# Optimization experiments

Measured on AMD Instinct MI355X. Metric: run time of the kernel, lower is better.

## Reference

```python
import jax, jax.numpy as jnp
import numpy as np

MID = 128
N_STAGES = 5  # 224 -> 110 -> 53 -> 25 -> 11 -> 4 (conv3 valid + maxpool3 s2)
EPS_SN = 1e-12


def conv2d(x, w, b, ):
    y = jax.lax.conv_general_dilated(x, w, (1, 1), [(0, 0), (0, 0)],
                                     dimension_numbers=('NCHW', 'OIHW', 'NCHW'))
    return y + b[None, :, None, None]


def maxpool3s2(x):
    return jax.lax.reduce_window(x, -jnp.inf, jax.lax.max,
                                 (1, 1, 3, 3), (1, 1, 2, 2), 'VALID')


def batchnorm(x, g, b, eps=1e-5):
    mu = x.mean(axis=(0, 2, 3), keepdims=True)
    var = x.var(axis=(0, 2, 3), keepdims=True)  # biased, training-mode BN
    return (x - mu) * jax.lax.rsqrt(var + eps) * g[None, :, None, None] + b[None, :, None, None]


def lrn(x, size, alpha=1e-4, beta=0.75, k=1.0):
    # matches F.local_response_norm: zero-padded channel window average of x^2
    sq = x * x
    pad_l, pad_r = size // 2, (size - 1) // 2
    p = jnp.pad(sq, ((0, 0), (pad_l, pad_r), (0, 0), (0, 0)))
    cs = jnp.cumsum(p, axis=1)
    cs = jnp.concatenate([jnp.zeros_like(cs[:, :1]), cs], axis=1)
    win = cs[:, size:] - cs[:, :-size]  # (N,C,H,W) windowed sums
    return x / (k + alpha * win / size) ** beta


def spectral_normalize(theta, u0, v0):
    # u,v carry sequentially across the batch, as in the original python loop
    def nrm(z):
        return z / jnp.maximum(jnp.linalg.norm(z), EPS_SN)

    def step(carry, W):
        u, v = carry
        for _ in range(4):
            v = nrm(W.T @ u)
            u = nrm(W @ v)
        sigma = u @ (W @ v)
        return (u, v), W / sigma

    _, out = jax.lax.scan(step, (u0, v0), theta)
    return out


def affine_grid(theta, H, W):
    # align_corners=False pixel-center normalized coords
    xs = (jnp.arange(W, dtype=theta.dtype) * 2 + 1) / W - 1
    ys = (jnp.arange(H, dtype=theta.dtype) * 2 + 1) / H - 1
    gy, gx = jnp.meshgrid(ys, xs, indexing='ij')
    base = jnp.stack([gx, gy, jnp.ones_like(gx)], axis=-1)  # (H,W,3)
    return jnp.einsum('nij,hwj->nhwi', theta, base)  # (N,H,W,2), last dim (x,y)


def _reflect(x, size):
    # reflection padding over [-0.5, size-0.5], then clip (align_corners=False)
    x = jnp.abs(x + 0.5) % (2.0 * size)
    x = jnp.where(x > size, 2.0 * size - x, x)
    return jnp.clip(x - 0.5, 0.0, size - 1.0)


def grid_sample_reflect(img, grid):
    N, C, H, W = img.shape
    ix = _reflect(((grid[..., 0] + 1) * W - 1) * 0.5, W)
    iy = _reflect(((grid[..., 1] + 1) * H - 1) * 0.5, H)
    x0 = jnp.floor(ix); y0 = jnp.floor(iy)
    wx = ix - x0; wy = iy - y0
    x0i = jnp.clip(x0.astype(jnp.int32), 0, W - 1)
    y0i = jnp.clip(y0.astype(jnp.int32), 0, H - 1)
    x1i = jnp.clip(x0.astype(jnp.int32) + 1, 0, W - 1)
    y1i = jnp.clip(y0.astype(jnp.int32) + 1, 0, H - 1)

    def one(im, y0i, x0i, y1i, x1i, wx, wy):  # im: (C,H,W)
        return (im[:, y0i, x0i] * ((1 - wx) * (1 - wy))[None]
                + im[:, y0i, x1i] * (wx * (1 - wy))[None]
                + im[:, y1i, x0i] * ((1 - wx) * wy)[None]
                + im[:, y1i, x1i] * (wx * wy)[None])

    return jax.vmap(one)(img, y0i, x0i, y1i, x1i, wx, wy)


def forward(x, conv0_w, conv0_b, convs_w, convs_b, bn_g, bn_b, Wr, br, u0, v0):
    N, C, H, W = x.shape
    xs = jax.nn.relu(batchnorm(conv2d(x, conv0_w, conv0_b), bn_g[0], bn_b[0]))
    for i in range(N_STAGES):
        xs = conv2d(xs, convs_w[i], convs_b[i])
        xs = maxpool3s2(xs)
        xs = jax.nn.relu(batchnorm(xs, bn_g[i + 1], bn_b[i + 1]))
    xs = lrn(xs, MID)
    xs = xs.reshape(N, -1)
    reg = xs @ Wr.T + br  # (N,7)
    theta = reg[:, 0:6].reshape(-1, 2, 3)
    m = jax.nn.sigmoid(reg[:, 6])
    theta = spectral_normalize(theta, u0, v0)
    grid = affine_grid(theta, H, W)
    xout = grid_sample_reflect(x, grid)
    return xout * m[:, None, None, None]


def setup_inputs() -> dict:
    key = jax.random.key(0)
    ks = jax.random.split(key, 12)
    N, C, H, W = 16, 16, 224, 224
    x = jax.random.normal(ks[0], (N, C, H, W), dtype=jnp.float32)
    conv0_w = jax.random.normal(ks[1], (MID, C, 1, 1), dtype=jnp.float32) * 0.05
    conv0_b = jax.random.normal(ks[2], (MID,), dtype=jnp.float32) * 0.01
    convs_w = jax.random.normal(ks[3], (N_STAGES, MID, MID, 3, 3), dtype=jnp.float32) * 0.03
    convs_b = jax.random.normal(ks[4], (N_STAGES, MID), dtype=jnp.float32) * 0.01
    bn_g = jnp.ones((N_STAGES + 1, MID), dtype=jnp.float32)
    bn_b = jnp.zeros((N_STAGES + 1, MID), dtype=jnp.float32)
    feat = MID * 4 * 4  # final spatial 4x4
    Wr = jax.random.normal(ks[5], (7, feat), dtype=jnp.float32) * 0.01
    br = jnp.concatenate([jnp.array([1, 0, 0, 0, 1, 0], dtype=jnp.float32),
                          jax.random.normal(ks[6], (1,), dtype=jnp.float32) * 0.1])
    u0 = jax.random.normal(ks[7], (2,), dtype=jnp.float32)
    u0 = u0 / jnp.maximum(jnp.linalg.norm(u0), EPS_SN)
    v0 = jax.random.normal(ks[8], (3,), dtype=jnp.float32)
    v0 = v0 / jnp.maximum(jnp.linalg.norm(v0), EPS_SN)
    return {"x": x, "conv0_w": conv0_w, "conv0_b": conv0_b, "convs_w": convs_w,
            "convs_b": convs_b, "bn_g": bn_g, "bn_b": bn_b, "Wr": Wr, "br": br,
            "u0": u0, "v0": v0}


def reference(x, conv0_w, conv0_b, convs_w, convs_b, bn_g, bn_b, Wr, br, u0, v0):
    return forward(x, conv0_w, conv0_b, convs_w, convs_b, bn_g, bn_b, Wr, br, u0, v0)
```

## Files before the change

kernel.cpp:

```cpp
#include <hip/hip_runtime.h>
#include <math.h>


#define CO_PB 8
#define PLANE 1216

__device__ __forceinline__ void gld_lds4(const float* g, float* l) {
  __builtin_amdgcn_global_load_lds(
      (const __attribute__((address_space(1))) void*)(g),
      (__attribute__((address_space(3))) void*)(l), 4, 0, 0);
}

__global__ void zero_kernel(float* __restrict__ p, int n) {
  int i = blockIdx.x * 256 + threadIdx.x;
  if (i < n) p[i] = 0.f;
}

__global__ __launch_bounds__(256) void moment_kernel(
    const float* __restrict__ x, float* __restrict__ mom) {
  const int tid = threadIdx.x;
  int q = blockIdx.x * 256 + tid;
  int n = q / 12544, pq = q - n * 12544;
  const float* xb = x + ((long)n * 16) * 50176 + pq * 4;
  float4 v4[16];
#pragma unroll
  for (int i = 0; i < 16; ++i) v4[i] = *(const float4*)(xb + (long)i * 50176);
  float accs[16];
  float accp[136];
#pragma unroll
  for (int i = 0; i < 16; ++i) accs[i] = 0.f;
#pragma unroll
  for (int k = 0; k < 136; ++k) accp[k] = 0.f;
#pragma unroll
  for (int p = 0; p < 4; ++p) {
    float v[16];
#pragma unroll
    for (int i = 0; i < 16; ++i)
      v[i] = (p == 0) ? v4[i].x : (p == 1) ? v4[i].y : (p == 2) ? v4[i].z : v4[i].w;
#pragma unroll
    for (int i = 0; i < 16; ++i) accs[i] += v[i];
    int k = 0;
#pragma unroll
    for (int i = 0; i < 16; ++i)
#pragma unroll
      for (int j = i; j < 16; ++j) { accp[k] += v[i] * v[j]; ++k; }
  }
  __shared__ float s_part[4][152];
  const int lane = tid & 63, wv = tid >> 6;
#pragma unroll
  for (int k = 0; k < 16; ++k) {
    float t = accs[k];
#pragma unroll
    for (int o = 32; o; o >>= 1) t += __shfl_down(t, o, 64);
    if (lane == 0) s_part[wv][k] = t;
  }
#pragma unroll
  for (int k = 0; k < 136; ++k) {
    float t = accp[k];
#pragma unroll
    for (int o = 32; o; o >>= 1) t += __shfl_down(t, o, 64);
    if (lane == 0) s_part[wv][16 + k] = t;
  }
  __syncthreads();
  if (tid < 152) {
    float t = s_part[0][tid] + s_part[1][tid] + s_part[2][tid] + s_part[3][tid];
    atomicAdd(&mom[tid], t);
  }
}

__global__ void foldbn_kernel(const float* __restrict__ w0,
                              const float* __restrict__ mom,
                              const float* __restrict__ g,
                              const float* __restrict__ b,
                              float* __restrict__ Wp, float* __restrict__ bp) {
  int c = threadIdx.x;
  if (c >= 128) return;
  const float invN = 1.f / 802816.f;
  float w[16], m[16];
#pragma unroll
  for (int i = 0; i < 16; ++i) { w[i] = w0[c * 16 + i]; m[i] = mom[i] * invN; }
  float mu = 0.f;
#pragma unroll
  for (int i = 0; i < 16; ++i) mu += w[i] * m[i];
  float ey2 = 0.f;
  int k = 0;
#pragma unroll
  for (int i = 0; i < 16; ++i)
#pragma unroll
    for (int j = i; j < 16; ++j) {
      float Mij = mom[16 + k] * invN;
      ey2 += ((i == j) ? 1.f : 2.f) * w[i] * w[j] * Mij;
      ++k;
    }
  float var = ey2 - mu * mu;
  float al = g[c] * rsqrtf(var + 1e-5f);
#pragma unroll
  for (int i = 0; i < 16; ++i) Wp[c * 16 + i] = al * w[i];
  bp[c] = b[c] - al * mu;
}

__global__ __launch_bounds__(256) void conv0act_kernel(
    const float* __restrict__ x, const float* __restrict__ Wp,
    const float* __restrict__ bp, float* __restrict__ act, int n_base) {
  __shared__ float sw[512];
  __shared__ float sb[32];
  const int tid = threadIdx.x;
  const int co0 = blockIdx.y * 32;
  for (int e = tid; e < 512; e += 256) sw[e] = Wp[co0 * 16 + e];
  if (tid < 32) sb[tid] = bp[co0 + tid];
  __syncthreads();
  const int q = blockIdx.x * 256 + tid;
  const int nloc = blockIdx.z;
  const float* xb = x + ((long)(n_base + nloc) * 16) * 50176 + q * 4;
  float4 v4[16];
#pragma unroll
  for (int i = 0; i < 16; ++i) v4[i] = *(const float4*)(xb + (long)i * 50176);
  float* ob = act + ((long)nloc * 128) * 50176 + q * 4;
  for (int u = 0; u < 32; ++u) {
    float bb = sb[u];
    float4 a = make_float4(bb, bb, bb, bb);
#pragma unroll
    for (int i = 0; i < 16; ++i) {
      float w = sw[u * 16 + i];
      a.x += w * v4[i].x; a.y += w * v4[i].y;
      a.z += w * v4[i].z; a.w += w * v4[i].w;
    }
    a.x = fmaxf(a.x, 0.f); a.y = fmaxf(a.y, 0.f);
    a.z = fmaxf(a.z, 0.f); a.w = fmaxf(a.w, 0.f);
    *(float4*)(ob + (long)(co0 + u) * 50176) = a;
  }
}

__global__ __launch_bounds__(256) void stats_kernel(
    const float* __restrict__ buf, float* __restrict__ stats, int P2) {
  const int c = blockIdx.x;
  const int n = blockIdx.y;
  const int tid = threadIdx.x;
  const float* b = buf + ((long)n * 128 + c) * P2;
  float s = 0.f, q = 0.f;
  for (int i = tid; i < P2; i += 256) {
    float v = b[i];
    s += v; q += v * v;
  }
  __shared__ float rs[256], rq[256];
  rs[tid] = s; rq[tid] = q;
  __syncthreads();
  for (int off = 128; off; off >>= 1) {
    if (tid < off) { rs[tid] += rs[tid + off]; rq[tid] += rq[tid + off]; }
    __syncthreads();
  }
  if (tid == 0) {
    atomicAdd(&stats[c], rs[0]);
    atomicAdd(&stats[128 + c], rq[0]);
  }
}

__global__ __launch_bounds__(256) void bnrelu_kernel(
    float* __restrict__ buf, const float* __restrict__ stats,
    const float* __restrict__ g, const float* __restrict__ b,
    int P2, float invM, long total) {
  long i = (long)blockIdx.x * 256 + threadIdx.x;
  if (i >= total) return;
  int c = (int)((i / P2) & 127);
  float mu = stats[c] * invM;
  float var = stats[128 + c] * invM - mu * mu;
  float al = g[c] * rsqrtf(var + 1e-5f);
  float v = buf[i];
  buf[i] = fmaxf(al * (v - mu) + b[c], 0.f);
}

__global__ __launch_bounds__(256, 4) void conv3pool_kernel(
    const float* __restrict__ in, const float* __restrict__ wt,
    float* __restrict__ out, int Sin, int Pout, int n_base) {
  const int tid = threadIdx.x;
  const int tilesX = (Pout + 14) / 15;
  const int ty = blockIdx.x / tilesX, tx = blockIdx.x - ty * tilesX;
  const int co0 = blockIdx.y * CO_PB;
  const int nloc = blockIdx.z;
  const int py0 = ty * 15, px0 = tx * 15;
  const int iy0 = py0 * 2, ix0 = px0 * 2;

  __shared__ __align__(16) float s_in[4 * PLANE];
  __shared__ __align__(16) float s_wt[4][CO_PB][12];

  const int pi = tid >> 4, pj = tid & 15;

  int off[5];
#pragma unroll
  for (int j = 0; j < 5; ++j) {
    int e2 = tid + 256 * j;
    int r = e2 / 34, cc = e2 - 34 * r;
    int gy = iy0 + r; if (gy > Sin - 1) gy = Sin - 1;
    int gx = ix0 + cc; if (gx > Sin - 1) gx = Sin - 1;
    off[j] = gy * Sin + gx;
  }

  int wg0, wl0, wg1, wl1;
  {
    int e = tid;
    int cil = e / 72, rem = e - 72 * cil, u = rem / 9, t = rem - 9 * u;
    wg0 = ((co0 + u) * 128 + cil) * 9 + t;
    wl0 = (cil * CO_PB + u) * 12 + t;
    e = tid + 256;
    cil = e / 72; rem = e - 72 * cil; u = rem / 9; t = rem - 9 * u;
    wg1 = ((co0 + u) * 128 + cil) * 9 + t;
    wl1 = (cil * CO_PB + u) * 12 + t;
  }

  float acc[CO_PB][4];
#pragma unroll
  for (int u = 0; u < CO_PB; ++u)
#pragma unroll
    for (int k = 0; k < 4; ++k) acc[u][k] = 0.f;

  const long S2 = (long)Sin * Sin;
  const float* inN = in + ((long)nloc * 128) * S2;
  const int wb = tid & 192;

  for (int ci0 = 0; ci0 < 128; ci0 += 4) {
    __syncthreads();

    float w0v = wt[wg0 + 9 * ci0];
    float w1v = 0.f;
    if (tid < 32) w1v = wt[wg1 + 9 * ci0];

#pragma unroll
    for (int cil = 0; cil < 4; ++cil) {
      const float* src = inN + (long)(ci0 + cil) * S2;
      float* dplane = &s_in[cil * PLANE + wb];
#pragma unroll
      for (int j = 0; j < 4; ++j) gld_lds4(src + off[j], dplane + j * 256);
      if (tid < 192) gld_lds4(src + off[4], dplane + 4 * 256);
    }

    ((float*)s_wt)[wl0] = w0v;
    if (tid < 32) ((float*)s_wt)[wl1] = w1v;
    __syncthreads();

#pragma unroll
    for (int cil = 0; cil < 4; ++cil) {
      const float* ip = &s_in[cil * PLANE] + (2 * pi) * 34 + 2 * pj;
      float iv[16];
#pragma unroll
      for (int r = 0; r < 4; ++r) {
        float2 a = *(const float2*)(ip + r * 34);
        float2 b = *(const float2*)(ip + r * 34 + 2);
        iv[r * 4 + 0] = a.x; iv[r * 4 + 1] = a.y;
        iv[r * 4 + 2] = b.x; iv[r * 4 + 3] = b.y;
      }
#pragma unroll
      for (int u = 0; u < CO_PB; ++u) {
        const float4* wq = (const float4*)&s_wt[cil][u][0];
        float4 q0 = wq[0], q1 = wq[1], q2 = wq[2];
        float wv[9] = {q0.x, q0.y, q0.z, q0.w, q1.x, q1.y, q1.z, q1.w, q2.x};
#pragma unroll
        for (int ky = 0; ky < 3; ++ky)
#pragma unroll
          for (int kx = 0; kx < 3; ++kx) {
            float w = wv[ky * 3 + kx];
            acc[u][0] += w * iv[ky * 4 + kx];
            acc[u][1] += w * iv[ky * 4 + kx + 1];
            acc[u][2] += w * iv[(ky + 1) * 4 + kx];
            acc[u][3] += w * iv[(ky + 1) * 4 + kx + 1];
          }
      }
    }
  }

  float* s_conv = s_in;
  const int gpy = py0 + pi, gpx = px0 + pj;
  const bool wvalid = (pi < 15) && (pj < 15) && (gpy < Pout) && (gpx < Pout);
  float* cp = s_conv + (2 * pi) * 33 + 2 * pj;
  const float* rp = s_conv + (2 * pi) * 33 + 2 * pj;
#pragma unroll
  for (int u = 0; u < CO_PB; ++u) {
    __syncthreads();
    cp[0] = acc[u][0]; cp[1] = acc[u][1];
    cp[33] = acc[u][2]; cp[34] = acc[u][3];
    __syncthreads();
    if (wvalid) {
      float mx = rp[0];
#pragma unroll
      for (int dy = 0; dy < 3; ++dy)
#pragma unroll
        for (int dx = 0; dx < 3; ++dx)
          mx = fmaxf(mx, rp[dy * 33 + dx]);
      out[(((long)(n_base + nloc) * 128 + (co0 + u)) * Pout + gpy) * Pout + gpx] = mx;
    }
  }
}

__global__ __launch_bounds__(128) void lrn_kernel(float* __restrict__ buf) {
  const int n = blockIdx.x;
  const int c = threadIdx.x;
  __shared__ float sq[128];
  float* b = buf + (long)n * 2048;
  for (int p = 0; p < 16; ++p) {
    float v = b[c * 16 + p];
    sq[c] = v * v;
    __syncthreads();
    int lo = c - 64 < 0 ? 0 : c - 64;
    int hi = c + 63 > 127 ? 127 : c + 63;
    float win = 0.f;
    for (int j = lo; j <= hi; ++j) win += sq[j];
    b[c * 16 + p] = v * powf(1.f + (1e-4f / 128.f) * win, -0.75f);
    __syncthreads();
  }
}

__global__ __launch_bounds__(256) void gemv_kernel(
    const float* __restrict__ xs, const float* __restrict__ Wr,
    const float* __restrict__ br, float* __restrict__ reg) {
  const int n = blockIdx.x;
  const int tid = threadIdx.x;
  float a[7] = {0.f, 0.f, 0.f, 0.f, 0.f, 0.f, 0.f};
  for (int e = tid; e < 2048; e += 256) {
    float v = xs[(long)n * 2048 + e];
#pragma unroll
    for (int j = 0; j < 7; ++j) a[j] += v * Wr[j * 2048 + e];
  }
  __shared__ float red[256];
  for (int j = 0; j < 7; ++j) {
    red[tid] = a[j];
    __syncthreads();
    for (int off = 128; off; off >>= 1) {
      if (tid < off) red[tid] += red[tid + off];
      __syncthreads();
    }
    if (tid == 0) reg[n * 7 + j] = red[0] + br[j];
    __syncthreads();
  }
}

__global__ void sn_kernel(const float* __restrict__ reg,
                          const float* __restrict__ u0g,
                          const float* __restrict__ v0g,
                          float* __restrict__ theta, float* __restrict__ m) {
  if (threadIdx.x != 0 || blockIdx.x != 0) return;
  float u[2] = {u0g[0], u0g[1]};
  float v[3] = {v0g[0], v0g[1], v0g[2]};
  for (int n = 0; n < 16; ++n) {
    const float* W = reg + n * 7;
    for (int it = 0; it < 4; ++it) {
      float v0n = W[0] * u[0] + W[3] * u[1];
      float v1n = W[1] * u[0] + W[4] * u[1];
      float v2n = W[2] * u[0] + W[5] * u[1];
      float nv = sqrtf(v0n * v0n + v1n * v1n + v2n * v2n);
      nv = fmaxf(nv, 1e-12f);
      v[0] = v0n / nv; v[1] = v1n / nv; v[2] = v2n / nv;
      float u0n = W[0] * v[0] + W[1] * v[1] + W[2] * v[2];
      float u1n = W[3] * v[0] + W[4] * v[1] + W[5] * v[2];
      float nu = sqrtf(u0n * u0n + u1n * u1n);
      nu = fmaxf(nu, 1e-12f);
      u[0] = u0n / nu; u[1] = u1n / nu;
    }
    float Wv0 = W[0] * v[0] + W[1] * v[1] + W[2] * v[2];
    float Wv1 = W[3] * v[0] + W[4] * v[1] + W[5] * v[2];
    float sigma = u[0] * Wv0 + u[1] * Wv1;
    for (int k = 0; k < 6; ++k) theta[n * 6 + k] = W[k] / sigma;
    m[n] = 1.f / (1.f + expf(-W[6]));
  }
}

__device__ __forceinline__ float reflectf(float x, float size) {
  x = fabsf(x + 0.5f);
  x = fmodf(x, 2.f * size);
  if (x > size) x = 2.f * size - x;
  x -= 0.5f;
  return fminf(fmaxf(x, 0.f), size - 1.f);
}

__global__ __launch_bounds__(256) void sample_kernel(
    const float* __restrict__ x, const float* __restrict__ theta,
    const float* __restrict__ m, float* __restrict__ out) {
  long i = (long)blockIdx.x * 256 + threadIdx.x;
  if (i >= 12845056L) return;
  int w = (int)(i % 224);
  long t = i / 224;
  int h = (int)(t % 224); t /= 224;
  int c = (int)(t % 16);
  int n = (int)(t / 16);
  const float* th = theta + n * 6;
  float xn = (2 * w + 1) * (1.f / 224.f) - 1.f;
  float yn = (2 * h + 1) * (1.f / 224.f) - 1.f;
  float gx = th[0] * xn + th[1] * yn + th[2];
  float gy = th[3] * xn + th[4] * yn + th[5];
  float ix = reflectf(((gx + 1.f) * 224.f - 1.f) * 0.5f, 224.f);
  float iy = reflectf(((gy + 1.f) * 224.f - 1.f) * 0.5f, 224.f);
  float x0 = floorf(ix), y0 = floorf(iy);
  float wx = ix - x0, wy = iy - y0;
  int x0i = (int)x0; if (x0i < 0) x0i = 0; if (x0i > 223) x0i = 223;
  int y0i = (int)y0; if (y0i < 0) y0i = 0; if (y0i > 223) y0i = 223;
  int x1i = (int)x0 + 1; if (x1i < 0) x1i = 0; if (x1i > 223) x1i = 223;
  int y1i = (int)y0 + 1; if (y1i < 0) y1i = 0; if (y1i > 223) y1i = 223;
  const float* im = x + ((long)n * 16 + c) * 50176;
  float v00 = im[y0i * 224 + x0i], v01 = im[y0i * 224 + x1i];
  float v10 = im[y1i * 224 + x0i], v11 = im[y1i * 224 + x1i];
  float val = v00 * (1.f - wx) * (1.f - wy) + v01 * wx * (1.f - wy) +
              v10 * (1.f - wx) * wy + v11 * wx * wy;
  out[i] = val * m[n];
}

extern "C" void kernel_launch(void* const* d_in, const int* in_sizes, int n_in,
                              void* d_out, int out_size, void* d_ws,
                              size_t ws_size, hipStream_t stream) {
  const float* x       = (const float*)d_in[0];
  const float* conv0_w = (const float*)d_in[1];
  const float* convs_w = (const float*)d_in[3];
  const float* bn_g = (const float*)d_in[5];
  const float* bn_b = (const float*)d_in[6];
  const float* Wr   = (const float*)d_in[7];
  const float* br   = (const float*)d_in[8];
  const float* u0   = (const float*)d_in[9];
  const float* v0   = (const float*)d_in[10];
  float* out = (float*)d_out;
  float* ws  = (float*)d_ws;

  float* bufB   = ws;
  float* stats  = ws + 24780800L;
  float* mom    = stats + 256;
  float* Wp     = mom + 160;
  float* bp     = Wp + 2048;
  float* regb   = bp + 128;
  float* thetab = regb + 112;
  float* mb     = thetab + 96;

  float* tempAct = out;
  float* bufC    = out;

  zero_kernel<<<2, 256, 0, stream>>>(stats, 416);
  moment_kernel<<<784, 256, 0, stream>>>(x, mom);
  foldbn_kernel<<<1, 128, 0, stream>>>(conv0_w, mom, bn_g, bn_b, Wp, bp);

  for (int r = 0; r < 8; ++r) {
    conv0act_kernel<<<dim3(49, 4, 2), 256, 0, stream>>>(x, Wp, bp, tempAct,
                                                        2 * r);
    conv3pool_kernel<<<dim3(64, 16, 2), 256, 0, stream>>>(
        tempAct, convs_w, bufB, 224, 110, 2 * r);
  }
  zero_kernel<<<1, 256, 0, stream>>>(stats, 256);
  stats_kernel<<<dim3(128, 16), 256, 0, stream>>>(bufB, stats, 12100);
  {
    long total = 16L * 128 * 12100;
    bnrelu_kernel<<<(int)((total + 255) / 256), 256, 0, stream>>>(
        bufB, stats, bn_g + 128, bn_b + 128, 12100, 1.f / (16.f * 12100.f),
        total);
  }

  const int Sins[4]  = {110, 53, 25, 11};
  const int Pouts[4] = {53, 25, 11, 4};
  for (int s = 0; s < 4; ++s) {
    float* ib = (s % 2 == 0) ? bufB : bufC;
    float* ob = (s % 2 == 0) ? bufC : bufB;
    int Sin = Sins[s], Pout = Pouts[s];
    int tiles = (Pout + 14) / 15;
    conv3pool_kernel<<<dim3(tiles * tiles, 16, 16), 256, 0, stream>>>(
        ib, convs_w + (long)(s + 1) * 128 * 128 * 9, ob, Sin, Pout, 0);
    zero_kernel<<<1, 256, 0, stream>>>(stats, 256);
    int P2 = Pout * Pout;
    stats_kernel<<<dim3(128, 16), 256, 0, stream>>>(ob, stats, P2);
    long total = 16L * 128 * P2;
    bnrelu_kernel<<<(int)((total + 255) / 256), 256, 0, stream>>>(
        ob, stats, bn_g + (s + 2) * 128, bn_b + (s + 2) * 128, P2,
        1.f / (16.f * P2), total);
  }

  lrn_kernel<<<16, 128, 0, stream>>>(bufB);
  gemv_kernel<<<16, 256, 0, stream>>>(bufB, Wr, br, regb);
  sn_kernel<<<1, 1, 0, stream>>>(regb, u0, v0, thetab, mb);
  sample_kernel<<<50176, 256, 0, stream>>>(x, thetab, mb, out);
}
```

Measured before the change: 7.638 ms.

## Fuse BN statistics into conv epilogue and BN+ReLU into next conv load

Conv3+pool epilogue now reduces per-channel sum and sum of squares with wave shuffles and double atomics, replacing separate stats kernels. The following conv applies the previous BN affine and ReLU while staging inputs into LDS, using a small bnprep kernel that computes the per-channel scale, mean and shift. This removes full read/write passes over activations for stats and bnrelu. The async global-to-LDS loads are replaced with register loads plus LDS stores, which may cost some load latency, and double atomics add contention.

```diff
diff --git a/kernel.cpp b/kernel.cpp
--- a/kernel.cpp
+++ b/kernel.cpp
@@ -3,13 +3,7 @@
 
 
 #define CO_PB 8
-#define PLANE 1216
-
-__device__ __forceinline__ void gld_lds4(const float* g, float* l) {
-  __builtin_amdgcn_global_load_lds(
-      (const __attribute__((address_space(1))) void*)(g),
-      (__attribute__((address_space(3))) void*)(l), 4, 0, 0);
-}
+#define PLANE 1156
 
 __global__ void zero_kernel(float* __restrict__ p, int n) {
   int i = blockIdx.x * 256 + threadIdx.x;
@@ -97,6 +91,22 @@
 #pragma unroll
   for (int i = 0; i < 16; ++i) Wp[c * 16 + i] = al * w[i];
   bp[c] = b[c] - al * mu;
+}
+
+__global__ void bnprep_kernel(const double* __restrict__ stats,
+                              const float* __restrict__ g,
+                              const float* __restrict__ b,
+                              double invM, float* __restrict__ bnab) {
+  int c = threadIdx.x;
+  if (c >= 128) return;
+  double mud = stats[c] * invM;
+  double qd = stats[128 + c] * invM;
+  float mu = (float)mud;
+  float var = (float)(qd - mud * mud);
+  float al = g[c] * rsqrtf(var + 1e-5f);
+  bnab[c] = al;
+  bnab[128 + c] = mu;
+  bnab[256 + c] = b[c];
 }
 
 __global__ __launch_bounds__(256) void conv0act_kernel(
@@ -131,39 +141,17 @@
   }
 }
 
-__global__ __launch_bounds__(256) void stats_kernel(
-    const float* __restrict__ buf, float* __restrict__ stats, int P2) {
-  const int c = blockIdx.x;
-  const int n = blockIdx.y;
-  const int tid = threadIdx.x;
-  const float* b = buf + ((long)n * 128 + c) * P2;
-  float s = 0.f, q = 0.f;
-  for (int i = tid; i < P2; i += 256) {
-    float v = b[i];
-    s += v; q += v * v;
-  }
-  __shared__ float rs[256], rq[256];
-  rs[tid] = s; rq[tid] = q;
-  __syncthreads();
-  for (int off = 128; off; off >>= 1) {
-    if (tid < off) { rs[tid] += rs[tid + off]; rq[tid] += rq[tid + off]; }
-    __syncthreads();
-  }
-  if (tid == 0) {
-    atomicAdd(&stats[c], rs[0]);
-    atomicAdd(&stats[128 + c], rq[0]);
-  }
-}
-
 __global__ __launch_bounds__(256) void bnrelu_kernel(
-    float* __restrict__ buf, const float* __restrict__ stats,
+    float* __restrict__ buf, const double* __restrict__ stats,
     const float* __restrict__ g, const float* __restrict__ b,
-    int P2, float invM, long total) {
+    int P2, double invM, long total) {
   long i = (long)blockIdx.x * 256 + threadIdx.x;
   if (i >= total) return;
   int c = (int)((i / P2) & 127);
-  float mu = stats[c] * invM;
-  float var = stats[128 + c] * invM - mu * mu;
+  double mud = stats[c] * invM;
+  double qd = stats[128 + c] * invM;
+  float mu = (float)mud;
+  float var = (float)(qd - mud * mud);
   float al = g[c] * rsqrtf(var + 1e-5f);
   float v = buf[i];
   buf[i] = fmaxf(al * (v - mu) + b[c], 0.f);
@@ -171,7 +159,8 @@
 
 __global__ __launch_bounds__(256, 4) void conv3pool_kernel(
     const float* __restrict__ in, const float* __restrict__ wt,
-    float* __restrict__ out, int Sin, int Pout, int n_base) {
+    float* __restrict__ out, int Sin, int Pout, int n_base,
+    const float* __restrict__ bnab, double* __restrict__ stats) {
   const int tid = threadIdx.x;
   const int tilesX = (Pout + 14) / 15;
   const int ty = blockIdx.x / tilesX, tx = blockIdx.x - ty * tilesX;
@@ -215,24 +204,45 @@
 
   const long S2 = (long)Sin * Sin;
   const float* inN = in + ((long)nloc * 128) * S2;
-  const int wb = tid & 192;
+  const bool dobn = (bnab != nullptr);
 
   for (int ci0 = 0; ci0 < 128; ci0 += 4) {
-    __syncthreads();
-
-    float w0v = wt[wg0 + 9 * ci0];
-    float w1v = 0.f;
-    if (tid < 32) w1v = wt[wg1 + 9 * ci0];
-
+    float al[4], mu[4], bb[4];
+#pragma unroll
+    for (int cil = 0; cil < 4; ++cil) {
+      al[cil] = dobn ? bnab[ci0 + cil] : 1.f;
+      mu[cil] = dobn ? bnab[128 + ci0 + cil] : 0.f;
+      bb[cil] = dobn ? bnab[256 + ci0 + cil] : 0.f;
+    }
+    float sv[4][5];
 #pragma unroll
     for (int cil = 0; cil < 4; ++cil) {
       const float* src = inN + (long)(ci0 + cil) * S2;
-      float* dplane = &s_in[cil * PLANE + wb];
-#pragma unroll
-      for (int j = 0; j < 4; ++j) gld_lds4(src + off[j], dplane + j * 256);
-      if (tid < 192) gld_lds4(src + off[4], dplane + 4 * 256);
-    }
-
+#pragma unroll
+      for (int j = 0; j < 4; ++j) sv[cil][j] = src[off[j]];
+      sv[cil][4] = (tid < 132) ? src[off[4]] : 0.f;
+    }
+    float w0v = wt[wg0 + 9 * ci0];
+    float w1v = (tid < 32) ? wt[wg1 + 9 * ci0] : 0.f;
+
+    __syncthreads();
+#pragma unroll
+    for (int cil = 0; cil < 4; ++cil) {
+      if (dobn) {
+#pragma unroll
+        for (int j = 0; j < 4; ++j)
+          s_in[cil * PLANE + tid + 256 * j] =
+              fmaxf(al[cil] * (sv[cil][j] - mu[cil]) + bb[cil], 0.f);
+        if (tid < 132)
+          s_in[cil * PLANE + tid + 1024] =
+              fmaxf(al[cil] * (sv[cil][4] - mu[cil]) + bb[cil], 0.f);
+      } else {
+#pragma unroll
+        for (int j = 0; j < 4; ++j)
+          s_in[cil * PLANE + tid + 256 * j] = sv[cil][j];
+        if (tid < 132) s_in[cil * PLANE + tid + 1024] = sv[cil][4];
+      }
+    }
     ((float*)s_wt)[wl0] = w0v;
     if (tid < 32) ((float*)s_wt)[wl1] = w1v;
     __syncthreads();
@@ -278,14 +288,26 @@
     cp[0] = acc[u][0]; cp[1] = acc[u][1];
     cp[33] = acc[u][2]; cp[34] = acc[u][3];
     __syncthreads();
+    float mx = 0.f;
     if (wvalid) {
-      float mx = rp[0];
+      mx = rp[0];
 #pragma unroll
       for (int dy = 0; dy < 3; ++dy)
 #pragma unroll
         for (int dx = 0; dx < 3; ++dx)
           mx = fmaxf(mx, rp[dy * 33 + dx]);
       out[(((long)(n_base + nloc) * 128 + (co0 + u)) * Pout + gpy) * Pout + gpx] = mx;
+    }
+    float s = wvalid ? mx : 0.f;
+    float q = wvalid ? mx * mx : 0.f;
+#pragma unroll
+    for (int o = 32; o; o >>= 1) {
+      s += __shfl_down(s, o, 64);
+      q += __shfl_down(q, o, 64);
+    }
+    if ((tid & 63) == 0) {
+      atomicAdd(&stats[co0 + u], (double)s);
+      atomicAdd(&stats[128 + co0 + u], (double)q);
     }
   }
 }
@@ -416,53 +438,60 @@
   float* out = (float*)d_out;
   float* ws  = (float*)d_ws;
 
-  float* bufB   = ws;
-  float* stats  = ws + 24780800L;
-  float* mom    = stats + 256;
-  float* Wp     = mom + 160;
-  float* bp     = Wp + 2048;
-  float* regb   = bp + 128;
-  float* thetab = regb + 112;
-  float* mb     = thetab + 96;
+  float* bufB = ws;
+  double* statsD = (double*)(ws + 24780800L);
+  float* mom = (float*)statsD;
+  float* Wp  = ws + 24781312L;
+  float* bp  = ws + 24783360L;
+
+  float* bnab2 = Wp;
+  float* bnab3 = Wp + 384;
+  float* bnab4 = Wp + 768;
+  float* bnab5 = Wp + 1152;
+  float* regb   = Wp + 1536;
+  float* thetab = Wp + 1648;
+  float* mb     = Wp + 1744;
 
   float* tempAct = out;
   float* bufC    = out;
 
-  zero_kernel<<<2, 256, 0, stream>>>(stats, 416);
+  zero_kernel<<<2, 256, 0, stream>>>((float*)statsD, 512);
   moment_kernel<<<784, 256, 0, stream>>>(x, mom);
   foldbn_kernel<<<1, 128, 0, stream>>>(conv0_w, mom, bn_g, bn_b, Wp, bp);
+  zero_kernel<<<2, 256, 0, stream>>>((float*)statsD, 512);
 
   for (int r = 0; r < 8; ++r) {
     conv0act_kernel<<<dim3(49, 4, 2), 256, 0, stream>>>(x, Wp, bp, tempAct,
                                                         2 * r);
     conv3pool_kernel<<<dim3(64, 16, 2), 256, 0, stream>>>(
-        tempAct, convs_w, bufB, 224, 110, 2 * r);
-  }
-  zero_kernel<<<1, 256, 0, stream>>>(stats, 256);
-  stats_kernel<<<dim3(128, 16), 256, 0, stream>>>(bufB, stats, 12100);
-  {
-    long total = 16L * 128 * 12100;
-    bnrelu_kernel<<<(int)((total + 255) / 256), 256, 0, stream>>>(
-        bufB, stats, bn_g + 128, bn_b + 128, 12100, 1.f / (16.f * 12100.f),
-        total);
-  }
+        tempAct, convs_w, bufB, 224, 110, 2 * r, nullptr, statsD);
+  }
+  bnprep_kernel<<<1, 128, 0, stream>>>(statsD, bn_g + 128, bn_b + 128,
+                                       1.0 / (16.0 * 12100.0), bnab2);
 
   const int Sins[4]  = {110, 53, 25, 11};
   const int Pouts[4] = {53, 25, 11, 4};
+  float* bnabs[4] = {bnab2, bnab3, bnab4, bnab5};
   for (int s = 0; s < 4; ++s) {
     float* ib = (s % 2 == 0) ? bufB : bufC;
     float* ob = (s % 2 == 0) ? bufC : bufB;
     int Sin = Sins[s], Pout = Pouts[s];
     int tiles = (Pout + 14) / 15;
+    zero_kernel<<<2, 256, 0, stream>>>((float*)statsD, 512);
     conv3pool_kernel<<<dim3(tiles * tiles, 16, 16), 256, 0, stream>>>(
-        ib, convs_w + (long)(s + 1) * 128 * 128 * 9, ob, Sin, Pout, 0);
-    zero_kernel<<<1, 256, 0, stream>>>(stats, 256);
+        ib, convs_w + (long)(s + 1) * 128 * 128 * 9, ob, Sin, Pout, 0,
+        bnabs[s], statsD);
     int P2 = Pout * Pout;
-    stats_kernel<<<dim3(128, 16), 256, 0, stream>>>(ob, stats, P2);
-    long total = 16L * 128 * P2;
-    bnrelu_kernel<<<(int)((total + 255) / 256), 256, 0, stream>>>(
-        ob, stats, bn_g + (s + 2) * 128, bn_b + (s + 2) * 128, P2,
-        1.f / (16.f * P2), total);
+    if (s < 3) {
+      bnprep_kernel<<<1, 128, 0, stream>>>(statsD, bn_g + (s + 2) * 128,
+                                           bn_b + (s + 2) * 128,
+                                           1.0 / (16.0 * P2), bnabs[s + 1]);
+    } else {
+      long total = 16L * 128 * P2;
+      bnrelu_kernel<<<(int)((total + 255) / 256), 256, 0, stream>>>(
+          bufB, statsD, bn_g + (s + 2) * 128, bn_b + (s + 2) * 128, P2,
+          1.0 / (16.0 * P2), total);
+    }
   }
 
   lrn_kernel<<<16, 128, 0, stream>>>(bufB);
```

Result: slower. 17.71 ms (+131.8%).

## Double-buffer conv3pool input and weight tiles with async global-to-LDS prefetch

Applied to the files above, without the earlier changes.

The conv3pool kernel now keeps two LDS buffers for the input planes and the weights. It issues the global_load_lds transfers for the next 4-channel chunk before computing on the current one, and uses explicit vmcnt waits plus raw s_barrier in place of __syncthreads. The aim is to hide global memory latency behind the FMA work. In exchange LDS use roughly doubles, which may cut occupancy below the launch_bounds target of 4 blocks. The hand-written waitcnt values, and the loads that all threads now issue (the tid<192 and tid<32 guards are gone), need to be correct for the result to stay valid.

```diff
diff --git a/kernel.cpp b/kernel.cpp
--- a/kernel.cpp
+++ b/kernel.cpp
@@ -3,7 +3,7 @@
 
 
 #define CO_PB 8
-#define PLANE 1216
+#define PLANE 1280
 
 __device__ __forceinline__ void gld_lds4(const float* g, float* l) {
   __builtin_amdgcn_global_load_lds(
@@ -180,8 +180,8 @@
   const int py0 = ty * 15, px0 = tx * 15;
   const int iy0 = py0 * 2, ix0 = px0 * 2;
 
-  __shared__ __align__(16) float s_in[4 * PLANE];
-  __shared__ __align__(16) float s_wt[4][CO_PB][12];
+  __shared__ __align__(16) float s_in[2][4 * PLANE];
+  __shared__ __align__(16) float s_wt[2][4][CO_PB][12];
 
   const int pi = tid >> 4, pj = tid & 15;
 
@@ -217,29 +217,41 @@
   const float* inN = in + ((long)nloc * 128) * S2;
   const int wb = tid & 192;
 
+  auto issue_dma = [&](int c0, int b) {
+#pragma unroll
+    for (int cil = 0; cil < 4; ++cil) {
+      const float* src = inN + (long)(c0 + cil) * S2;
+      float* dp = &s_in[b][cil * PLANE + wb];
+#pragma unroll
+      for (int j = 0; j < 5; ++j) gld_lds4(src + off[j], dp + j * 256);
+    }
+  };
+
+  issue_dma(0, 0);
+  float w0v = wt[wg0];
+  float w1v = wt[wg1];
+
   for (int ci0 = 0; ci0 < 128; ci0 += 4) {
-    __syncthreads();
-
-    float w0v = wt[wg0 + 9 * ci0];
-    float w1v = 0.f;
-    if (tid < 32) w1v = wt[wg1 + 9 * ci0];
+    const int cur = (ci0 >> 2) & 1;
+    float w0n = 0.f, w1n = 0.f;
+    if (ci0 < 124) {
+      issue_dma(ci0 + 4, cur ^ 1);
+      w0n = wt[wg0 + 9 * (ci0 + 4)];
+      w1n = wt[wg1 + 9 * (ci0 + 4)];
+      asm volatile("s_waitcnt vmcnt(22)" ::: "memory");
+    } else {
+      asm volatile("s_waitcnt vmcnt(0)" ::: "memory");
+    }
+    __builtin_amdgcn_sched_barrier(0);
+    ((float*)&s_wt[cur][0][0][0])[wl0] = w0v;
+    if (tid < 32) ((float*)&s_wt[cur][0][0][0])[wl1] = w1v;
+    asm volatile("s_waitcnt lgkmcnt(0)" ::: "memory");
+    __builtin_amdgcn_sched_barrier(0);
+    __builtin_amdgcn_s_barrier();
 
 #pragma unroll
     for (int cil = 0; cil < 4; ++cil) {
-      const float* src = inN + (long)(ci0 + cil) * S2;
-      float* dplane = &s_in[cil * PLANE + wb];
-#pragma unroll
-      for (int j = 0; j < 4; ++j) gld_lds4(src + off[j], dplane + j * 256);
-      if (tid < 192) gld_lds4(src + off[4], dplane + 4 * 256);
-    }
-
-    ((float*)s_wt)[wl0] = w0v;
-    if (tid < 32) ((float*)s_wt)[wl1] = w1v;
-    __syncthreads();
-
-#pragma unroll
-    for (int cil = 0; cil < 4; ++cil) {
-      const float* ip = &s_in[cil * PLANE] + (2 * pi) * 34 + 2 * pj;
+      const float* ip = &s_in[cur][cil * PLANE] + (2 * pi) * 34 + 2 * pj;
       float iv[16];
 #pragma unroll
       for (int r = 0; r < 4; ++r) {
@@ -250,7 +262,7 @@
       }
 #pragma unroll
       for (int u = 0; u < CO_PB; ++u) {
-        const float4* wq = (const float4*)&s_wt[cil][u][0];
+        const float4* wq = (const float4*)&s_wt[cur][cil][u][0];
         float4 q0 = wq[0], q1 = wq[1], q2 = wq[2];
         float wv[9] = {q0.x, q0.y, q0.z, q0.w, q1.x, q1.y, q1.z, q1.w, q2.x};
 #pragma unroll
@@ -265,9 +277,11 @@
           }
       }
     }
-  }
-
-  float* s_conv = s_in;
+    __builtin_amdgcn_s_barrier();
+    w0v = w0n; w1v = w1n;
+  }
+
+  float* s_conv = &s_in[0][0];
   const int gpy = py0 + pi, gpx = px0 + pj;
   const bool wvalid = (pi < 15) && (pj < 15) && (gpy < Pout) && (gpx < Pout);
   float* cp = s_conv + (2 * pi) * 33 + 2 * pj;
```

After: 6.680 ms. 12.5% less time.
